# Kernel optimization log

Measured on AMD Instinct MI355X. Metric: run time of the kernel, lower is better.

## Reference

```python
import jax, jax.numpy as jnp
import numpy as np
from jax import lax


def _conv2d(x, w, b):
    # x: [B,C,H,W], w: [O,I,3,3], 'SAME' padding, stride 1
    y = lax.conv_general_dilated(x, w, (1, 1), 'SAME',
                                 dimension_numbers=('NCHW', 'OIHW', 'NCHW'))
    return y + b[None, :, None, None]


def _grid_sample_border(img, grid):
    # img: [B,C,H,W]; grid: [B,H,W,2] with (x,y) in [-1,1]; align_corners=True,
    # bilinear, padding_mode='border' (coords clamped before interpolation).
    B, C, H, W = img.shape
    ix = jnp.clip((grid[..., 0] + 1.0) * (W - 1) / 2.0, 0.0, W - 1.0)
    iy = jnp.clip((grid[..., 1] + 1.0) * (H - 1) / 2.0, 0.0, H - 1.0)
    x0f = jnp.floor(ix)
    y0f = jnp.floor(iy)
    wx = (ix - x0f)[:, None]  # [B,1,H,W]
    wy = (iy - y0f)[:, None]
    x0 = jnp.clip(x0f.astype(jnp.int32), 0, W - 1)
    x1 = jnp.clip(x0 + 1, 0, W - 1)
    y0 = jnp.clip(y0f.astype(jnp.int32), 0, H - 1)
    y1 = jnp.clip(y0 + 1, 0, H - 1)
    flat = img.reshape(B, C, H * W)

    def gather(yi, xi):
        idx = (yi * W + xi).reshape(B, 1, H * W)
        g = jnp.take_along_axis(flat, jnp.broadcast_to(idx, (B, C, H * W)), axis=2)
        return g.reshape(B, C, H, W)

    v00 = gather(y0, x0)
    v01 = gather(y0, x1)
    v10 = gather(y1, x0)
    v11 = gather(y1, x1)
    top = v00 * (1.0 - wx) + v01 * wx
    bot = v10 * (1.0 - wx) + v11 * wx
    return top * (1.0 - wy) + bot * wy


def setup_inputs() -> dict:
    key = jax.random.key(0)
    ks = jax.random.split(key, 4)
    B, C, H, W = 4, 64, 256, 256
    z_real = jax.random.normal(ks[0], (B, C, H, W), dtype=jnp.float32)
    z_imag = jax.random.normal(ks[1], (B, C, H, W), dtype=jnp.float32)
    fan1 = C * 9
    w1 = jax.random.normal(ks[2], (64, C, 3, 3), dtype=jnp.float32) / np.sqrt(fan1)
    b1 = jnp.zeros((64,), dtype=jnp.float32)
    w2 = jax.random.normal(ks[3], (1, 64, 3, 3), dtype=jnp.float32) / np.sqrt(64 * 9)
    b2 = jnp.zeros((1,), dtype=jnp.float32)
    dt = jnp.float32(0.1)
    return {"z_real": z_real, "z_imag": z_imag, "dt": dt,
            "w1": w1, "b1": b1, "w2": w2, "b2": b2}


def reference(z_real, z_imag, dt, w1, b1, w2, b2):
    B, C, H, W = z_real.shape
    # psi_net: conv -> SiLU -> conv, scaled by dt; psi: [B,1,H,W]
    psi = _conv2d(jax.nn.silu(_conv2d(z_real, w1, b1)), w2, b2) * dt
    # curl with replicate padding, central differences
    p = jnp.pad(psi, ((0, 0), (0, 0), (1, 1), (1, 1)), mode='edge')
    u = (p[:, :, 2:, 1:-1] - p[:, :, :-2, 1:-1]) / 2.0
    v = -(p[:, :, 1:-1, 2:] - p[:, :, 1:-1, :-2]) / 2.0
    # normalized flow: [B,H,W,2]
    flow = jnp.concatenate([u / (W / 2.0), v / (H / 2.0)], axis=1).transpose(0, 2, 3, 1)
    yy, xx = jnp.meshgrid(jnp.linspace(-1.0, 1.0, H), jnp.linspace(-1.0, 1.0, W), indexing='ij')
    base = jnp.stack((xx, yy), axis=-1).astype(z_real.dtype)  # [H,W,2]
    sampling_grid = base[None] - flow
    # sample real and imag in one fused gather over 2C channels
    zc = jnp.concatenate([z_real, z_imag], axis=1)  # [B,2C,H,W]
    out = _grid_sample_border(zc, sampling_grid)
    return out  # [B,2C,H,W]: first C channels = real part, last C = imag part
```

## Files before the change

kernel.cpp:

```cpp
#include <hip/hip_runtime.h>
#include <cmath>

namespace {
constexpr int H = 256, W = 256, HWp = H * W;
constexpr size_t PLANE = (size_t)4 * HWp * 64 * 2;
constexpr size_t NEED_FAST = 73728 + 2 * PLANE + (1u << 20);
}

typedef _Float16 f16;
typedef unsigned int u32;
typedef __attribute__((ext_vector_type(4))) _Float16 f16x4;
typedef __attribute__((ext_vector_type(8))) _Float16 f16x8;
typedef __attribute__((ext_vector_type(4))) float f32x4;
typedef __attribute__((ext_vector_type(4))) unsigned int u32x4;

__device__ __forceinline__ void dma16(const char* g, char* l) {
    __builtin_amdgcn_global_load_lds(
        (const __attribute__((address_space(1))) u32*)g,
        (__attribute__((address_space(3))) u32*)l, 16, 0, 0);
}

__global__ __launch_bounds__(256) void k_xt2(const float* __restrict__ zr,
                                             const float* __restrict__ zi,
                                             f16* __restrict__ Xt_r,
                                             f16* __restrict__ Xt_i,
                                             const float* __restrict__ w1,
                                             f16* __restrict__ w1tb,
                                             int ny_xt) {
    if ((int)blockIdx.y == ny_xt) {
        int i = blockIdx.x * 256 + threadIdx.x;
        if (i < 64 * 576) {
            int co = i / 576, r = i - co * 576;
            int ci = r / 9, k9 = r - ci * 9;
            w1tb[(k9 * 64 + co) * 64 + ci] = (f16)w1[i];
        }
        return;
    }
    __shared__ f16 tile[64][80];
    const int t = threadIdx.x;
    const int p0 = blockIdx.x * 64;
    const int bb = blockIdx.y & 3;
    const bool im = blockIdx.y >= 4;
    const float* x = im ? zi : zr;
    f16* dst = im ? Xt_i : Xt_r;
    const size_t base = (size_t)bb * 64 * HWp;
#pragma unroll
    for (int r = 0; r < 4; ++r) {
        int q = r * 256 + t;
        int ci = q >> 4, px4 = (q & 15) * 4;
        f32x4 v = *reinterpret_cast<const f32x4*>(x + base + (size_t)ci * HWp + p0 + px4);
#pragma unroll
        for (int j = 0; j < 4; ++j) tile[px4 + j][ci] = (f16)v[j];
    }
    __syncthreads();
    const int px = t >> 2, q = t & 3;
    u32x4* d = reinterpret_cast<u32x4*>(dst + ((size_t)bb * HWp + p0 + px) * 64 + q * 16);
    const u32x4* s = reinterpret_cast<const u32x4*>(&tile[px][q * 16]);
    d[0] = s[0];
    d[1] = s[1];
}

__global__ __launch_bounds__(256, 2) void k_conv1(
        const f16* __restrict__ Xt,
        const f16* __restrict__ w1tb,
        const float* __restrict__ b1,
        f16* __restrict__ act) {
    __shared__ __align__(16) char lds[18432];

    const int tid = threadIdx.x;
    const int lane = tid & 63, wid = tid >> 6;
    const int lr = lane & 15, lg = lane >> 4;
    const int wpx = wid & 1, wco = wid >> 1;

    const int bid = blockIdx.x;
    const int swz = (bid & 7) * 256 + (bid >> 3);
    const int b = swz >> 9;
    const int y = (swz >> 1) & 255;
    const int x0 = (swz & 1) << 7;

    const int swzb = (lane ^ ((lane >> 3) & 7)) << 4;

    f16x8 Wreg[9][2][2];
#pragma unroll
    for (int k9 = 0; k9 < 9; ++k9)
#pragma unroll
        for (int n = 0; n < 2; ++n)
#pragma unroll
            for (int c = 0; c < 2; ++c)
                Wreg[k9][n][c] = *reinterpret_cast<const f16x8*>(
                    w1tb + (size_t)(k9 * 64 + wco * 32 + n * 16 + lr) * 64
                         + c * 32 + lg * 8);

    f32x4 acc[4][2];
#pragma unroll
    for (int m = 0; m < 4; ++m)
#pragma unroll
        for (int n = 0; n < 2; ++n) acc[m][n] = (f32x4)0.f;

    const f16x8 zf = (f16x8)(f16)0.f;

#pragma unroll
    for (int dyi = 0; dyi < 3; ++dyi) {
        const int yy = y + dyi - 1;
        if ((unsigned)yy >= 256u) continue;

        __syncthreads();
        {
            const char* asrc = (const char*)Xt +
                ((((size_t)b * 256 + yy) * 256 + x0 - 8) * 128) + swzb;
#pragma unroll
            for (int j = 0; j < 5; ++j) {
                const int jj = wid + j * 4;
                if (jj < 18) dma16(asrc + jj * 1024, lds + jj * 1024);
            }
        }
        __syncthreads();

#pragma unroll
        for (int kx = 0; kx < 3; ++kx) {
            const int dx = kx - 1;
            const int gx0 = x0 + wpx * 64 + lr + dx;
            const bool ok0 = (unsigned)gx0 < 256u;
            const bool ok3 = (unsigned)(gx0 + 48) < 256u;
            const int arow = (8 + wpx * 64 + lr + dx) << 7;
            const int axor = (lr + dx) & 7;
#pragma unroll
            for (int c = 0; c < 2; ++c) {
                const int abase = arow + (((c * 4 + lg) ^ axor) << 4);
                f16x8 A0 = *reinterpret_cast<const f16x8*>(lds + abase);
                f16x8 A1 = *reinterpret_cast<const f16x8*>(lds + abase + 2048);
                f16x8 A2 = *reinterpret_cast<const f16x8*>(lds + abase + 4096);
                f16x8 A3 = *reinterpret_cast<const f16x8*>(lds + abase + 6144);
                A0 = ok0 ? A0 : zf;
                A3 = ok3 ? A3 : zf;
                const f16x8 W0 = Wreg[dyi * 3 + kx][0][c];
                const f16x8 W1 = Wreg[dyi * 3 + kx][1][c];
                acc[0][0] = __builtin_amdgcn_mfma_f32_16x16x32_f16(W0, A0, acc[0][0], 0, 0, 0);
                acc[0][1] = __builtin_amdgcn_mfma_f32_16x16x32_f16(W1, A0, acc[0][1], 0, 0, 0);
                acc[1][0] = __builtin_amdgcn_mfma_f32_16x16x32_f16(W0, A1, acc[1][0], 0, 0, 0);
                acc[1][1] = __builtin_amdgcn_mfma_f32_16x16x32_f16(W1, A1, acc[1][1], 0, 0, 0);
                acc[2][0] = __builtin_amdgcn_mfma_f32_16x16x32_f16(W0, A2, acc[2][0], 0, 0, 0);
                acc[2][1] = __builtin_amdgcn_mfma_f32_16x16x32_f16(W1, A2, acc[2][1], 0, 0, 0);
                acc[3][0] = __builtin_amdgcn_mfma_f32_16x16x32_f16(W0, A3, acc[3][0], 0, 0, 0);
                acc[3][1] = __builtin_amdgcn_mfma_f32_16x16x32_f16(W1, A3, acc[3][1], 0, 0, 0);
            }
        }
    }

    float bias[2][4];
#pragma unroll
    for (int n = 0; n < 2; ++n) {
        f32x4 bv = *reinterpret_cast<const f32x4*>(b1 + wco * 32 + n * 16 + lg * 4);
#pragma unroll
        for (int r = 0; r < 4; ++r) bias[n][r] = bv[r];
    }
    const size_t row_base = ((size_t)b * 256 + y) * 256;
#pragma unroll
    for (int m = 0; m < 4; ++m) {
        f16* ap = act + (row_base + x0 + wpx * 64 + m * 16 + lr) * 64 + wco * 32 + lg * 4;
#pragma unroll
        for (int n = 0; n < 2; ++n) {
            f16x4 o;
#pragma unroll
            for (int r = 0; r < 4; ++r) {
                float v = acc[m][n][r] + bias[n][r];
                v = v / (1.f + __expf(-v));
                o[r] = (f16)v;
            }
            *reinterpret_cast<f16x4*>(ap + n * 16) = o;
        }
    }
}

__global__ __launch_bounds__(256) void k_conv2(
        const f16* __restrict__ act, const float* __restrict__ w2,
        const float* __restrict__ b2, const float* __restrict__ dtp,
        float* __restrict__ psi) {
    const int tx = threadIdx.x & 31, ty = threadIdx.x >> 5;
    const int px = blockIdx.x * 32 + tx;
    const int py = blockIdx.y * 8 + ty;
    const int b = blockIdx.z;

    float a0 = 0.f, a1 = 0.f, a2 = 0.f, a3 = 0.f;
#pragma unroll
    for (int dy = -1; dy <= 1; ++dy) {
        const int yy = py + dy;
        if ((unsigned)yy >= (unsigned)H) continue;
#pragma unroll
        for (int dx = -1; dx <= 1; ++dx) {
            const int xx = px + dx;
            const int k9 = (dy + 1) * 3 + (dx + 1);
            if ((unsigned)xx < (unsigned)W) {
                const f16x8* ap = reinterpret_cast<const f16x8*>(
                    act + (((size_t)b * H + yy) * W + xx) * 64);
                const float* wp = w2 + k9;
#pragma unroll
                for (int g = 0; g < 8; ++g) {
                    const f16x8 v = ap[g];
                    const int cb = g * 8;
                    a0 = fmaf((float)v[0], wp[(cb + 0) * 9], a0);
                    a1 = fmaf((float)v[1], wp[(cb + 1) * 9], a1);
                    a2 = fmaf((float)v[2], wp[(cb + 2) * 9], a2);
                    a3 = fmaf((float)v[3], wp[(cb + 3) * 9], a3);
                    a0 = fmaf((float)v[4], wp[(cb + 4) * 9], a0);
                    a1 = fmaf((float)v[5], wp[(cb + 5) * 9], a1);
                    a2 = fmaf((float)v[6], wp[(cb + 6) * 9], a2);
                    a3 = fmaf((float)v[7], wp[(cb + 7) * 9], a3);
                }
            }
        }
    }
    psi[((size_t)b * H + py) * W + px] = ((a0 + a1) + (a2 + a3) + b2[0]) * dtp[0];
}

__global__ __launch_bounds__(256, 4) void k_sample3(
        const f16* __restrict__ Xt_r, const f16* __restrict__ Xt_i,
        const float* __restrict__ psi, float* __restrict__ out) {
    __shared__ int   s_off[4][128];
    __shared__ float s_w[4][128];
    __shared__ __align__(16) float s_stage[64][132];

    const int tid = threadIdx.x;
    const int bid = blockIdx.x;
    const int swz = (bid & 7) * 256 + (bid >> 3);
    const int seg = swz & 1, y = (swz >> 1) & 255, b = swz >> 9;
    const int x0 = seg * 128;

    if (tid < 128) {
        const int px = x0 + tid;
        const float* pb = psi + b * HWp;
        const int yp = min(y + 1, H - 1), ym = max(y - 1, 0);
        const int xp = min(px + 1, W - 1), xm = max(px - 1, 0);
        const float u = 0.5f * (pb[yp * W + px] - pb[ym * W + px]);
        const float v = -0.5f * (pb[y * W + xp] - pb[y * W + xm]);
        const float gx = (-1.f + 2.f * px / (float)(W - 1)) - u * (2.f / (float)W);
        const float gy = (-1.f + 2.f * y / (float)(H - 1)) - v * (2.f / (float)H);
        float ix = fminf(fmaxf((gx + 1.f) * 0.5f * (float)(W - 1), 0.f), (float)(W - 1));
        float iy = fminf(fmaxf((gy + 1.f) * 0.5f * (float)(H - 1), 0.f), (float)(H - 1));
        const float xf = floorf(ix), yf = floorf(iy);
        const float wx = ix - xf, wy = iy - yf;
        const int ix0 = (int)xf, iy0 = (int)yf;
        const int ix1 = min(ix0 + 1, W - 1), iy1 = min(iy0 + 1, H - 1);
        s_off[0][tid] = (iy0 * W + ix0) * 128;
        s_off[1][tid] = (iy0 * W + ix1) * 128;
        s_off[2][tid] = (iy1 * W + ix0) * 128;
        s_off[3][tid] = (iy1 * W + ix1) * 128;
        s_w[0][tid] = (1.f - wx) * (1.f - wy);
        s_w[1][tid] = wx * (1.f - wy);
        s_w[2][tid] = (1.f - wx) * wy;
        s_w[3][tid] = wx * wy;
    }
    __syncthreads();

    const int p = tid >> 1, s = tid & 1;
    const int o0 = s_off[0][p], o1 = s_off[1][p], o2 = s_off[2][p], o3 = s_off[3][p];
    const float w0 = s_w[0][p], w1 = s_w[1][p], w2 = s_w[2][p], w3 = s_w[3][p];
    const int cl = tid >> 5;
    const int pxq = (tid & 31) * 4;
    const size_t obase = (size_t)b * 128 * HWp + (size_t)y * W + x0 + pxq;

#pragma unroll
    for (int pl = 0; pl < 2; ++pl) {
        const char* base = (const char*)(pl ? Xt_i : Xt_r)
                         + (size_t)b * HWp * 128 + s * 64;
        const char* c0 = base + o0;
        const char* c1 = base + o1;
        const char* c2 = base + o2;
        const char* c3 = base + o3;
        f16x8 h00 = *(const f16x8*)(c0);      f16x8 h01 = *(const f16x8*)(c0 + 16);
        f16x8 h02 = *(const f16x8*)(c0 + 32); f16x8 h03 = *(const f16x8*)(c0 + 48);
        f16x8 h10 = *(const f16x8*)(c1);      f16x8 h11 = *(const f16x8*)(c1 + 16);
        f16x8 h12 = *(const f16x8*)(c1 + 32); f16x8 h13 = *(const f16x8*)(c1 + 48);
        f16x8 h20 = *(const f16x8*)(c2);      f16x8 h21 = *(const f16x8*)(c2 + 16);
        f16x8 h22 = *(const f16x8*)(c2 + 32); f16x8 h23 = *(const f16x8*)(c2 + 48);
        f16x8 h30 = *(const f16x8*)(c3);      f16x8 h31 = *(const f16x8*)(c3 + 16);
        f16x8 h32 = *(const f16x8*)(c3 + 32); f16x8 h33 = *(const f16x8*)(c3 + 48);

        const int rb = s << 5;
#pragma unroll
        for (int k = 0; k < 8; ++k) {
            s_stage[rb + k][p] = w0 * (float)h00[k] + w1 * (float)h10[k]
                               + w2 * (float)h20[k] + w3 * (float)h30[k];
            s_stage[rb + 8 + k][p] = w0 * (float)h01[k] + w1 * (float)h11[k]
                                   + w2 * (float)h21[k] + w3 * (float)h31[k];
            s_stage[rb + 16 + k][p] = w0 * (float)h02[k] + w1 * (float)h12[k]
                                    + w2 * (float)h22[k] + w3 * (float)h32[k];
            s_stage[rb + 24 + k][p] = w0 * (float)h03[k] + w1 * (float)h13[k]
                                    + w2 * (float)h23[k] + w3 * (float)h33[k];
        }
        __syncthreads();
#pragma unroll
        for (int k = 0; k < 8; ++k) {
            const int c = cl + (k << 3);
            f32x4 vv = *(const f32x4*)&s_stage[c][pxq];
            *(f32x4*)(out + obase + (size_t)(pl * 64 + c) * HWp) = vv;
        }
        __syncthreads();
    }
}

__global__ __launch_bounds__(256) void k_sample_fb(
        const float* __restrict__ zr, const float* __restrict__ zi,
        const float* __restrict__ psi, float* __restrict__ out) {
    const int tx = threadIdx.x & 31, ty = threadIdx.x >> 5;
    const int px = blockIdx.x * 32 + tx;
    const int py = blockIdx.y * 8 + ty;
    const int b  = blockIdx.z >> 3;
    const int c0 = (blockIdx.z & 7) * 16;

    const float* pb = psi + b * HWp;
    const int yp = min(py + 1, H - 1), ym = max(py - 1, 0);
    const int xp = min(px + 1, W - 1), xm = max(px - 1, 0);
    const float u = 0.5f * (pb[yp * W + px] - pb[ym * W + px]);
    const float v = -0.5f * (pb[py * W + xp] - pb[py * W + xm]);

    const float gx = (-1.f + 2.f * px / (float)(W - 1)) - u * (2.f / (float)W);
    const float gy = (-1.f + 2.f * py / (float)(H - 1)) - v * (2.f / (float)H);

    float ix = fminf(fmaxf((gx + 1.f) * 0.5f * (float)(W - 1), 0.f), (float)(W - 1));
    float iy = fminf(fmaxf((gy + 1.f) * 0.5f * (float)(H - 1), 0.f), (float)(H - 1));
    const float xf = floorf(ix), yf = floorf(iy);
    const float wx = ix - xf, wy = iy - yf;
    const int ix0 = (int)xf, iy0 = (int)yf;
    const int ix1 = min(ix0 + 1, W - 1), iy1 = min(iy0 + 1, H - 1);

    const int o00 = iy0 * W + ix0, o01 = iy0 * W + ix1;
    const int o10 = iy1 * W + ix0, o11 = iy1 * W + ix1;
    const float w00 = (1.f - wx) * (1.f - wy), w01 = wx * (1.f - wy);
    const float w10 = (1.f - wx) * wy, w11 = wx * wy;

    const float* src0 = (c0 < 64) ? (zr + (size_t)b * 64 * HWp + (size_t)c0 * HWp)
                                  : (zi + (size_t)b * 64 * HWp + (size_t)(c0 - 64) * HWp);
    float* ob = out + ((size_t)b * 128 + c0) * HWp + py * W + px;
#pragma unroll
    for (int c = 0; c < 16; ++c) {
        const float* p = src0 + (size_t)c * HWp;
        ob[(size_t)c * HWp] = p[o00] * w00 + p[o01] * w01 + p[o10] * w10 + p[o11] * w11;
    }
}

extern "C" void kernel_launch(void* const* d_in, const int* in_sizes, int n_in,
                              void* d_out, int out_size, void* d_ws, size_t ws_size,
                              hipStream_t stream) {
    const float* z_real = (const float*)d_in[0];
    const float* z_imag = (const float*)d_in[1];
    const float* dt     = (const float*)d_in[2];
    const float* w1     = (const float*)d_in[3];
    const float* b1     = (const float*)d_in[4];
    const float* w2     = (const float*)d_in[5];
    const float* b2     = (const float*)d_in[6];

    float* out = (float*)d_out;
    char* ws = (char*)d_ws;
    f16* w1tb = (f16*)ws;

    if (ws_size >= NEED_FAST) {
        f16* Xt_r  = (f16*)(ws + 73728);
        f16* Xt_i  = (f16*)(ws + 73728 + PLANE);
        float* psi = (float*)(ws + 73728 + 2 * PLANE);
        f16* act   = (f16*)d_out;

        hipLaunchKernelGGL(k_xt2, dim3(HWp / 64, 9), dim3(256), 0, stream,
                           z_real, z_imag, Xt_r, Xt_i, w1, w1tb, 8);
        hipLaunchKernelGGL(k_conv1, dim3(2048), dim3(256), 0, stream, Xt_r, w1tb, b1, act);
        hipLaunchKernelGGL(k_conv2, dim3(8, 32, 4), dim3(256), 0, stream, act, w2, b2, dt, psi);
        hipLaunchKernelGGL(k_sample3, dim3(2048), dim3(256), 0, stream,
                           Xt_r, Xt_i, psi, out);
    } else {
        float* psi = (float*)(ws + 73728);
        f16* Xt  = (f16*)((char*)d_out + 4096);
        f16* act = (f16*)((char*)d_out + 4096 + PLANE);

        hipLaunchKernelGGL(k_xt2, dim3(HWp / 64, 5), dim3(256), 0, stream,
                           z_real, z_real, Xt, Xt, w1, w1tb, 4);
        hipLaunchKernelGGL(k_conv1, dim3(2048), dim3(256), 0, stream, Xt, w1tb, b1, act);
        hipLaunchKernelGGL(k_conv2, dim3(8, 32, 4), dim3(256), 0, stream, act, w2, b2, dt, psi);
        hipLaunchKernelGGL(k_sample_fb, dim3(8, 32, 32), dim3(256), 0, stream,
                           z_real, z_imag, psi, out);
    }
}
```

Baseline: 169.6 us.

## Restructure conv1 into 4-row blocks with rolling LDS row buffer and prefetch

Each conv1 block now handles four full output rows of one image with 512 threads, instead of a 128-pixel half row. Input rows are staged once into a 4-slot LDS ring buffer (128 KB) and reused across the three kernel rows. The next row is prefetched via global_load_lds while the current row is computed. This is meant to cut redundant input loads and barrier stalls, at the cost of one block per CU, a grid of only 256 blocks, and a very large LDS footprint.

```diff
diff --git a/kernel.cpp b/kernel.cpp
--- a/kernel.cpp
+++ b/kernel.cpp
@@ -60,25 +60,25 @@
     d[1] = s[1];
 }
 
-__global__ __launch_bounds__(256, 2) void k_conv1(
+__global__ __launch_bounds__(512, 1) void k_conv1(
         const f16* __restrict__ Xt,
         const f16* __restrict__ w1tb,
         const float* __restrict__ b1,
         f16* __restrict__ act) {
-    __shared__ __align__(16) char lds[18432];
+    __shared__ __align__(16) char lds[131072];
 
     const int tid = threadIdx.x;
     const int lane = tid & 63, wid = tid >> 6;
     const int lr = lane & 15, lg = lane >> 4;
-    const int wpx = wid & 1, wco = wid >> 1;
+    const int pg = wid & 3, cg = wid >> 2;
 
     const int bid = blockIdx.x;
-    const int swz = (bid & 7) * 256 + (bid >> 3);
-    const int b = swz >> 9;
-    const int y = (swz >> 1) & 255;
-    const int x0 = (swz & 1) << 7;
+    const int swz = (bid & 7) * 32 + (bid >> 3);
+    const int b = swz >> 6;
+    const int y0 = (swz & 63) * 4;
 
     const int swzb = (lane ^ ((lane >> 3) & 7)) << 4;
+    const size_t img = (size_t)b * 256;
 
     f16x8 Wreg[9][2][2];
 #pragma unroll
@@ -88,87 +88,100 @@
 #pragma unroll
             for (int c = 0; c < 2; ++c)
                 Wreg[k9][n][c] = *reinterpret_cast<const f16x8*>(
-                    w1tb + (size_t)(k9 * 64 + wco * 32 + n * 16 + lr) * 64
+                    w1tb + (size_t)(k9 * 64 + cg * 32 + n * 16 + lr) * 64
                          + c * 32 + lg * 8);
 
-    f32x4 acc[4][2];
-#pragma unroll
-    for (int m = 0; m < 4; ++m)
-#pragma unroll
-        for (int n = 0; n < 2; ++n) acc[m][n] = (f32x4)0.f;
+    float bias[2][4];
+#pragma unroll
+    for (int n = 0; n < 2; ++n) {
+        f32x4 bv = *reinterpret_cast<const f32x4*>(b1 + cg * 32 + n * 16 + lg * 4);
+#pragma unroll
+        for (int r = 0; r < 4; ++r) bias[n][r] = bv[r];
+    }
+
+    auto stage = [&](int yy) {
+        const char* src = (const char*)Xt + ((img + yy) * 256) * 128 + swzb;
+        char* dst = lds + (yy & 3) * 32768;
+#pragma unroll
+        for (int i = 0; i < 4; ++i) {
+            const int ch = wid + i * 8;
+            dma16(src + ch * 1024, dst + ch * 1024);
+        }
+    };
+
+    if (y0 > 0) stage(y0 - 1);
+    stage(y0);
+    stage(y0 + 1);
+    __syncthreads();
 
     const f16x8 zf = (f16x8)(f16)0.f;
 
-#pragma unroll
-    for (int dyi = 0; dyi < 3; ++dyi) {
-        const int yy = y + dyi - 1;
-        if ((unsigned)yy >= 256u) continue;
-
+    for (int r = 0; r < 4; ++r) {
+        const int y = y0 + r;
+        const int yn = y + 2;
+        if (r < 3 && yn < 256) stage(yn);
+
+        f32x4 acc[4][2];
+#pragma unroll
+        for (int m = 0; m < 4; ++m)
+#pragma unroll
+            for (int n = 0; n < 2; ++n) acc[m][n] = (f32x4)0.f;
+
+#pragma unroll
+        for (int dyi = 0; dyi < 3; ++dyi) {
+            const int yy = y + dyi - 1;
+            if ((unsigned)yy >= 256u) continue;
+            const char* sb = lds + (yy & 3) * 32768;
+#pragma unroll
+            for (int kx = 0; kx < 3; ++kx) {
+                const int dx = kx - 1;
+                const int px1 = pg * 64 + 16 + lr + dx;
+                const bool ok0 = (unsigned)(px1 - 16) < 256u;
+                const bool ok3 = (unsigned)(px1 + 32) < 256u;
+                const int px0 = ok0 ? px1 - 16 : px1 - 16 - dx;
+                const int px2 = px1 + 16;
+                const int px3 = ok3 ? px1 + 32 : px1 + 32 - dx;
+                const int k9 = dyi * 3 + kx;
+#pragma unroll
+                for (int c = 0; c < 2; ++c) {
+                    const int pe = c * 4 + lg;
+                    f16x8 A0 = *(const f16x8*)(sb + (px0 << 7) + ((pe ^ (px0 & 7)) << 4));
+                    f16x8 A1 = *(const f16x8*)(sb + (px1 << 7) + ((pe ^ (px1 & 7)) << 4));
+                    f16x8 A2 = *(const f16x8*)(sb + (px2 << 7) + ((pe ^ (px2 & 7)) << 4));
+                    f16x8 A3 = *(const f16x8*)(sb + (px3 << 7) + ((pe ^ (px3 & 7)) << 4));
+                    A0 = ok0 ? A0 : zf;
+                    A3 = ok3 ? A3 : zf;
+                    const f16x8 W0 = Wreg[k9][0][c];
+                    const f16x8 W1 = Wreg[k9][1][c];
+                    acc[0][0] = __builtin_amdgcn_mfma_f32_16x16x32_f16(W0, A0, acc[0][0], 0, 0, 0);
+                    acc[0][1] = __builtin_amdgcn_mfma_f32_16x16x32_f16(W1, A0, acc[0][1], 0, 0, 0);
+                    acc[1][0] = __builtin_amdgcn_mfma_f32_16x16x32_f16(W0, A1, acc[1][0], 0, 0, 0);
+                    acc[1][1] = __builtin_amdgcn_mfma_f32_16x16x32_f16(W1, A1, acc[1][1], 0, 0, 0);
+                    acc[2][0] = __builtin_amdgcn_mfma_f32_16x16x32_f16(W0, A2, acc[2][0], 0, 0, 0);
+                    acc[2][1] = __builtin_amdgcn_mfma_f32_16x16x32_f16(W1, A2, acc[2][1], 0, 0, 0);
+                    acc[3][0] = __builtin_amdgcn_mfma_f32_16x16x32_f16(W0, A3, acc[3][0], 0, 0, 0);
+                    acc[3][1] = __builtin_amdgcn_mfma_f32_16x16x32_f16(W1, A3, acc[3][1], 0, 0, 0);
+                }
+            }
+        }
+
+        const size_t rb = (img + y) * 256;
+#pragma unroll
+        for (int m = 0; m < 4; ++m) {
+            f16* ap = act + (rb + pg * 64 + m * 16 + lr) * 64 + cg * 32 + lg * 4;
+#pragma unroll
+            for (int n = 0; n < 2; ++n) {
+                f16x4 o;
+#pragma unroll
+                for (int q = 0; q < 4; ++q) {
+                    float v = acc[m][n][q] + bias[n][q];
+                    v = v / (1.f + __expf(-v));
+                    o[q] = (f16)v;
+                }
+                *reinterpret_cast<f16x4*>(ap + n * 16) = o;
+            }
+        }
         __syncthreads();
-        {
-            const char* asrc = (const char*)Xt +
-                ((((size_t)b * 256 + yy) * 256 + x0 - 8) * 128) + swzb;
-#pragma unroll
-            for (int j = 0; j < 5; ++j) {
-                const int jj = wid + j * 4;
-                if (jj < 18) dma16(asrc + jj * 1024, lds + jj * 1024);
-            }
-        }
-        __syncthreads();
-
-#pragma unroll
-        for (int kx = 0; kx < 3; ++kx) {
-            const int dx = kx - 1;
-            const int gx0 = x0 + wpx * 64 + lr + dx;
-            const bool ok0 = (unsigned)gx0 < 256u;
-            const bool ok3 = (unsigned)(gx0 + 48) < 256u;
-            const int arow = (8 + wpx * 64 + lr + dx) << 7;
-            const int axor = (lr + dx) & 7;
-#pragma unroll
-            for (int c = 0; c < 2; ++c) {
-                const int abase = arow + (((c * 4 + lg) ^ axor) << 4);
-                f16x8 A0 = *reinterpret_cast<const f16x8*>(lds + abase);
-                f16x8 A1 = *reinterpret_cast<const f16x8*>(lds + abase + 2048);
-                f16x8 A2 = *reinterpret_cast<const f16x8*>(lds + abase + 4096);
-                f16x8 A3 = *reinterpret_cast<const f16x8*>(lds + abase + 6144);
-                A0 = ok0 ? A0 : zf;
-                A3 = ok3 ? A3 : zf;
-                const f16x8 W0 = Wreg[dyi * 3 + kx][0][c];
-                const f16x8 W1 = Wreg[dyi * 3 + kx][1][c];
-                acc[0][0] = __builtin_amdgcn_mfma_f32_16x16x32_f16(W0, A0, acc[0][0], 0, 0, 0);
-                acc[0][1] = __builtin_amdgcn_mfma_f32_16x16x32_f16(W1, A0, acc[0][1], 0, 0, 0);
-                acc[1][0] = __builtin_amdgcn_mfma_f32_16x16x32_f16(W0, A1, acc[1][0], 0, 0, 0);
-                acc[1][1] = __builtin_amdgcn_mfma_f32_16x16x32_f16(W1, A1, acc[1][1], 0, 0, 0);
-                acc[2][0] = __builtin_amdgcn_mfma_f32_16x16x32_f16(W0, A2, acc[2][0], 0, 0, 0);
-                acc[2][1] = __builtin_amdgcn_mfma_f32_16x16x32_f16(W1, A2, acc[2][1], 0, 0, 0);
-                acc[3][0] = __builtin_amdgcn_mfma_f32_16x16x32_f16(W0, A3, acc[3][0], 0, 0, 0);
-                acc[3][1] = __builtin_amdgcn_mfma_f32_16x16x32_f16(W1, A3, acc[3][1], 0, 0, 0);
-            }
-        }
-    }
-
-    float bias[2][4];
-#pragma unroll
-    for (int n = 0; n < 2; ++n) {
-        f32x4 bv = *reinterpret_cast<const f32x4*>(b1 + wco * 32 + n * 16 + lg * 4);
-#pragma unroll
-        for (int r = 0; r < 4; ++r) bias[n][r] = bv[r];
-    }
-    const size_t row_base = ((size_t)b * 256 + y) * 256;
-#pragma unroll
-    for (int m = 0; m < 4; ++m) {
-        f16* ap = act + (row_base + x0 + wpx * 64 + m * 16 + lr) * 64 + wco * 32 + lg * 4;
-#pragma unroll
-        for (int n = 0; n < 2; ++n) {
-            f16x4 o;
-#pragma unroll
-            for (int r = 0; r < 4; ++r) {
-                float v = acc[m][n][r] + bias[n][r];
-                v = v / (1.f + __expf(-v));
-                o[r] = (f16)v;
-            }
-            *reinterpret_cast<f16x4*>(ap + n * 16) = o;
-        }
     }
 }
 
@@ -362,7 +375,7 @@
 
         hipLaunchKernelGGL(k_xt2, dim3(HWp / 64, 9), dim3(256), 0, stream,
                            z_real, z_imag, Xt_r, Xt_i, w1, w1tb, 8);
-        hipLaunchKernelGGL(k_conv1, dim3(2048), dim3(256), 0, stream, Xt_r, w1tb, b1, act);
+        hipLaunchKernelGGL(k_conv1, dim3(256), dim3(512), 0, stream, Xt_r, w1tb, b1, act);
         hipLaunchKernelGGL(k_conv2, dim3(8, 32, 4), dim3(256), 0, stream, act, w2, b2, dt, psi);
         hipLaunchKernelGGL(k_sample3, dim3(2048), dim3(256), 0, stream,
                            Xt_r, Xt_i, psi, out);
@@ -373,7 +386,7 @@
 
         hipLaunchKernelGGL(k_xt2, dim3(HWp / 64, 5), dim3(256), 0, stream,
                            z_real, z_real, Xt, Xt, w1, w1tb, 4);
-        hipLaunchKernelGGL(k_conv1, dim3(2048), dim3(256), 0, stream, Xt, w1tb, b1, act);
+        hipLaunchKernelGGL(k_conv1, dim3(256), dim3(512), 0, stream, Xt, w1tb, b1, act);
         hipLaunchKernelGGL(k_conv2, dim3(8, 32, 4), dim3(256), 0, stream, act, w2, b2, dt, psi);
         hipLaunchKernelGGL(k_sample_fb, dim3(8, 32, 32), dim3(256), 0, stream,
                            z_real, z_imag, psi, out);
```

New measurement: 159.9 us. 5.7% less time.
